# Kernel optimization log

Measured on AMD Instinct MI355X. Metric: run time of the kernel, lower is better.

## Reference

```python
import jax, jax.numpy as jnp
import numpy as np

V, J, NB, NP = 100000, 24, 10, 207
PARENT = np.array([-1, 0, 0, 0, 1, 2, 3, 4, 5, 6, 7, 8, 9, 9, 9, 12, 13, 14, 16, 17, 18, 19, 20, 21])


def setup_inputs() -> dict:
    key = jax.random.key(0)
    ks = jax.random.split(key, 9)
    return {
        "beta": jax.random.normal(ks[0], (NB,), jnp.float32),
        "pose": jax.random.normal(ks[1], (J, 3), jnp.float32),
        "trans": jax.random.normal(ks[2], (3,), jnp.float32),
        "shapedirs": jax.random.normal(ks[3], (V, 3, NB), jnp.float32),
        "v_template": jax.random.normal(ks[4], (V, 3), jnp.float32),
        "J_regressor": jax.random.uniform(ks[5], (J, V), jnp.float32),
        "posedirs": jax.random.normal(ks[6], (V, 3, NP), jnp.float32),
        "weights": jax.random.uniform(ks[7], (V, J), jnp.float32),
        "faces": jax.random.randint(ks[8], (200000, 3), 0, V, jnp.int32),
    }


def _rodrigues(r):
    # r: [N,3] axis-angle -> [N,3,3] rotation matrices
    theta = jnp.sqrt(jnp.sum(r * r, axis=1, keepdims=True)) + 1e-8  # [N,1]
    rh = r / theta
    c = jnp.cos(theta)[:, :, None]  # [N,1,1]
    s = jnp.sin(theta)[:, :, None]
    z = jnp.zeros_like(rh[:, 0])
    K = jnp.stack([z, -rh[:, 2], rh[:, 1],
                   rh[:, 2], z, -rh[:, 0],
                   -rh[:, 1], rh[:, 0], z], axis=1).reshape(-1, 3, 3)
    outer = rh[:, :, None] * rh[:, None, :]
    I = jnp.eye(3, dtype=r.dtype)
    return c * I + (1.0 - c) * outer + s * K


def _with_zeros(Rt):
    # [3,4] -> [4,4] homogeneous
    bottom = jnp.array([[0.0, 0.0, 0.0, 1.0]], dtype=Rt.dtype)
    return jnp.concatenate([Rt, bottom], axis=0)


def reference(beta, pose, trans, shapedirs, v_template, J_regressor, posedirs, weights, faces):
    # shape blending
    v_shaped = jnp.einsum('vdb,b->vd', shapedirs, beta) + v_template  # [V,3]
    Jts = J_regressor @ v_shaped  # [J,3]
    R = _rodrigues(pose)  # [J,3,3]
    # pose blending: lrotmin = (R[1:] - I).flatten(), length 207
    lrotmin = (R[1:] - jnp.eye(3, dtype=R.dtype)).reshape(-1)
    v_posed = v_shaped + jnp.einsum('vdp,p->vd', posedirs, lrotmin)
    # forward kinematics along the 24-joint chain
    G = [_with_zeros(jnp.concatenate([R[0], Jts[0][:, None]], axis=1))]
    for i in range(1, J):
        p = int(PARENT[i])
        loc = _with_zeros(jnp.concatenate([R[i], (Jts[i] - Jts[p])[:, None]], axis=1))
        G.append(G[p] @ loc)
    stacked = jnp.stack(G, axis=0)  # [J,4,4]
    Jh = jnp.concatenate([Jts, jnp.zeros((J, 1), dtype=Jts.dtype)], axis=1)  # [J,4]
    corr = stacked @ Jh[:, :, None]  # [J,4,1]
    A = stacked - jnp.concatenate([jnp.zeros((J, 4, 3), dtype=stacked.dtype), corr], axis=2)
    # LBS skinning
    T = jnp.einsum('vj,jab->vab', weights, A)  # [V,4,4]
    rest = jnp.concatenate([v_posed, jnp.ones((v_posed.shape[0], 1), dtype=v_posed.dtype)], axis=1)  # [V,4]
    v = jnp.einsum('vab,vb->va', T, rest)[:, :3]
    vertices = v + trans[None, :]
    return vertices, faces
```

## Files before the change

kernel.cpp:

```cpp
#include <hip/hip_runtime.h>

#define V_N 100000
#define J_N 24
#define NB_N 10
#define NP_N 207
#define FLAT_P 621
#define FACE_I 600000
#define CHUNKS 50
#define CHUNK_V 2000
#define K1_BLK 1172
#define F_BLK  587

__device__ __constant__ int PARENT_D[24] = {
    -1, 0, 0, 0, 1, 2, 3, 4, 5, 6, 7, 8, 9, 9, 9, 12, 13, 14, 16, 17, 18, 19, 20, 21
};

__device__ __forceinline__ float wave_sum64(float x) {
    float t;
    t = __int_as_float(__builtin_amdgcn_update_dpp(0, __float_as_int(x), 0x111, 0xf, 0xf, true)); x += t;
    t = __int_as_float(__builtin_amdgcn_update_dpp(0, __float_as_int(x), 0x112, 0xf, 0xf, true)); x += t;
    t = __int_as_float(__builtin_amdgcn_update_dpp(0, __float_as_int(x), 0x114, 0xf, 0xf, true)); x += t;
    t = __int_as_float(__builtin_amdgcn_update_dpp(0, __float_as_int(x), 0x118, 0xf, 0xf, true)); x += t;
    t = __int_as_float(__builtin_amdgcn_update_dpp(0, __float_as_int(x), 0x142, 0xa, 0xf, true)); x += t;
    t = __int_as_float(__builtin_amdgcn_update_dpp(0, __float_as_int(x), 0x143, 0xc, 0xf, true)); x += t;
    return __int_as_float(__builtin_amdgcn_readlane(__float_as_int(x), 63));
}

__global__ __launch_bounds__(256) void kA_shape_faces(const float* __restrict__ shapedirs,
                                                      const float* __restrict__ vtemp,
                                                      const float* __restrict__ beta,
                                                      float* __restrict__ vshaped,
                                                      const int4* __restrict__ faces4,
                                                      float* __restrict__ out) {
    int b = blockIdx.x;
    if (b < K1_BLK) {
        int i = b * 256 + threadIdx.x;
        if (i >= V_N * 3) return;
        const float2* sd2 = reinterpret_cast<const float2*>(shapedirs + (size_t)i * NB_N);
        float2 p0 = sd2[0], p1 = sd2[1], p2 = sd2[2], p3 = sd2[3], p4 = sd2[4];
        float acc = vtemp[i];
        acc += p0.x * beta[0] + p0.y * beta[1];
        acc += p1.x * beta[2] + p1.y * beta[3];
        acc += p2.x * beta[4] + p2.y * beta[5];
        acc += p3.x * beta[6] + p3.y * beta[7];
        acc += p4.x * beta[8] + p4.y * beta[9];
        vshaped[i] = acc;
    } else {
        int i = (b - K1_BLK) * 256 + threadIdx.x;
        if (i < FACE_I / 4) {
            int4 f = faces4[i];
            float4* fdst = reinterpret_cast<float4*>(out + 300000);
            fdst[i] = make_float4((float)f.x, (float)f.y, (float)f.z, (float)f.w);
        }
    }
}

__global__ __launch_bounds__(256) void kB_partial(const float* __restrict__ Jreg,
                                                  const float* __restrict__ vshaped,
                                                  float* __restrict__ partials) {
    int c = blockIdx.x, j = blockIdx.y;
    int t = threadIdx.x;
    const float* row = Jreg + (size_t)j * V_N + (size_t)c * CHUNK_V;
    const float* vs  = vshaped + (size_t)c * CHUNK_V * 3;
    float s0 = 0.f, s1 = 0.f, s2 = 0.f;
    for (int i = t; i < CHUNK_V; i += 256) {
        float w = row[i];
        s0 += w * vs[i * 3 + 0];
        s1 += w * vs[i * 3 + 1];
        s2 += w * vs[i * 3 + 2];
    }
    for (int off = 32; off > 0; off >>= 1) {
        s0 += __shfl_xor(s0, off, 64);
        s1 += __shfl_xor(s1, off, 64);
        s2 += __shfl_xor(s2, off, 64);
    }
    __shared__ float ls[3][4];
    int wv = t >> 6;
    if ((t & 63) == 0) { ls[0][wv] = s0; ls[1][wv] = s1; ls[2][wv] = s2; }
    __syncthreads();
    if (t == 0) {
        float* p = partials + (size_t)c * 72 + j * 3;
        p[0] = ls[0][0] + ls[0][1] + ls[0][2] + ls[0][3];
        p[1] = ls[1][0] + ls[1][1] + ls[1][2] + ls[1][3];
        p[2] = ls[2][0] + ls[2][1] + ls[2][2] + ls[2][3];
    }
}

__global__ __launch_bounds__(128) void kC_fk(const float* __restrict__ pose,
                                             const float* __restrict__ partials,
                                             float* __restrict__ ws_lrot,
                                             float* __restrict__ ws_A) {
    __shared__ float R[24][9];
    __shared__ float G[24][12];
    __shared__ float Jts[24][3];
    int t = threadIdx.x;
    if (t < 72) {
        float s = 0.f;
        #pragma unroll
        for (int c = 0; c < CHUNKS; ++c) s += partials[c * 72 + t];
        (&Jts[0][0])[t] = s;
    }
    if (t < 24) {
        float x = pose[t * 3 + 0], y = pose[t * 3 + 1], z = pose[t * 3 + 2];
        float th = sqrtf(x * x + y * y + z * z) + 1e-8f;
        float inv = 1.0f / th;
        float rx = x * inv, ry = y * inv, rz = z * inv;
        float c = cosf(th), s = sinf(th), ic = 1.0f - c;
        R[t][0] = c + ic * rx * rx;      R[t][1] = ic * rx * ry - s * rz;  R[t][2] = ic * rx * rz + s * ry;
        R[t][3] = ic * ry * rx + s * rz; R[t][4] = c + ic * ry * ry;       R[t][5] = ic * ry * rz - s * rx;
        R[t][6] = ic * rz * rx - s * ry; R[t][7] = ic * rz * ry + s * rx;  R[t][8] = c + ic * rz * rz;
    }
    __syncthreads();
    for (int f = t; f < 640; f += 128) {
        float val = 0.0f;
        if (f < FLAT_P) {
            int p = f % NP_N;
            int j = 1 + p / 9;
            int e = p % 9;
            val = R[j][e] - ((e == 0 || e == 4 || e == 8) ? 1.0f : 0.0f);
        }
        ws_lrot[f] = val;
    }
    if (t < 12) {
        int r = t >> 2, c = t & 3;
        G[0][t] = (c < 3) ? R[0][r * 3 + c] : Jts[0][r];
    }
    __syncthreads();
    for (int i = 1; i < J_N; ++i) {
        int p = PARENT_D[i];
        if (t < 12) {
            int r = t >> 2, c = t & 3;
            float sum = (c == 3) ? G[p][r * 4 + 3] : 0.0f;
            #pragma unroll
            for (int k = 0; k < 3; ++k) {
                float loc = (c < 3) ? R[i][k * 3 + c] : (Jts[i][k] - Jts[p][k]);
                sum += G[p][r * 4 + k] * loc;
            }
            G[i][t] = sum;
        }
        __syncthreads();
    }
    if (t < 72) {
        int j = t / 3, r = t % 3;
        float g0 = G[j][r * 4 + 0], g1 = G[j][r * 4 + 1], g2 = G[j][r * 4 + 2], g3 = G[j][r * 4 + 3];
        float corr = g0 * Jts[j][0] + g1 * Jts[j][1] + g2 * Jts[j][2];
        ws_A[j * 12 + r * 4 + 0] = g0;
        ws_A[j * 12 + r * 4 + 1] = g1;
        ws_A[j * 12 + r * 4 + 2] = g2;
        ws_A[j * 12 + r * 4 + 3] = g3 - corr;
    }
}

__global__ __launch_bounds__(256) void kD_main(const float* __restrict__ posedirs,
                                               const float* __restrict__ weights,
                                               const float* __restrict__ vshaped,
                                               const float* __restrict__ ws_lrot,
                                               const float* __restrict__ ws_A,
                                               const float* __restrict__ trans,
                                               float* __restrict__ out) {
    __shared__ float sL[640];
    __shared__ float sA[288];
    int tid = threadIdx.x;
    for (int i = tid; i < 640; i += 256) sL[i] = ws_lrot[i];
    for (int i = tid; i < 288; i += 256) sA[i] = ws_A[i];
    __syncthreads();

    int lane = tid & 63;
    int v = blockIdx.x * 4 + (tid >> 6);
    if (v >= V_N) return;

    const float* pd = posedirs + (size_t)v * FLAT_P;
    float a0 = 0.f, a1 = 0.f, a2 = 0.f;
    #pragma unroll
    for (int k = 0; k < 10; ++k) {
        int f = lane + k * 64;
        if (f < FLAT_P) {
            float val = pd[f] * sL[f];
            if (f < 207)      a0 += val;
            else if (f < 414) a1 += val;
            else              a2 += val;
        }
    }
    float vp0 = wave_sum64(a0) + vshaped[v * 3 + 0];
    float vp1 = wave_sum64(a1) + vshaped[v * 3 + 1];
    float vp2 = wave_sum64(a2) + vshaped[v * 3 + 2];

    float r0 = 0.f, r1 = 0.f, r2 = 0.f;
    if (lane < J_N) {
        float w = weights[(size_t)v * J_N + lane];
        const float* A = &sA[lane * 12];
        r0 = w * (A[0] * vp0 + A[1] * vp1 + A[2]  * vp2 + A[3]);
        r1 = w * (A[4] * vp0 + A[5] * vp1 + A[6]  * vp2 + A[7]);
        r2 = w * (A[8] * vp0 + A[9] * vp1 + A[10] * vp2 + A[11]);
    }
    float s0 = wave_sum64(r0);
    float s1 = wave_sum64(r1);
    float s2 = wave_sum64(r2);

    if (lane < 3) {
        float res = (lane == 0) ? s0 : (lane == 1) ? s1 : s2;
        out[v * 3 + lane] = res + trans[lane];
    }
}

extern "C" void kernel_launch(void* const* d_in, const int* in_sizes, int n_in,
                              void* d_out, int out_size, void* d_ws, size_t ws_size,
                              hipStream_t stream) {
    const float* beta      = (const float*)d_in[0];
    const float* pose      = (const float*)d_in[1];
    const float* trans     = (const float*)d_in[2];
    const float* shapedirs = (const float*)d_in[3];
    const float* v_template= (const float*)d_in[4];
    const float* J_reg     = (const float*)d_in[5];
    const float* posedirs  = (const float*)d_in[6];
    const float* weights   = (const float*)d_in[7];
    const int*   faces     = (const int*)d_in[8];

    float* out = (float*)d_out;

    float* ws       = (float*)d_ws;
    float* vshaped  = ws;
    float* ws_lrot  = ws + 300080;
    float* ws_A     = ws + 300720;
    float* partials = ws + 301008;

    kA_shape_faces<<<K1_BLK + F_BLK, 256, 0, stream>>>(shapedirs, v_template, beta, vshaped,
                                                       (const int4*)faces, out);
    kB_partial<<<dim3(CHUNKS, J_N), 256, 0, stream>>>(J_reg, vshaped, partials);
    kC_fk<<<1, 128, 0, stream>>>(pose, partials, ws_lrot, ws_A);
    kD_main<<<(V_N + 3) / 4, 256, 0, stream>>>(posedirs, weights, vshaped, ws_lrot, ws_A, trans, out);
}
```

Baseline: 84.87 us.

## Split pose-blend and skinning into separate thread-per-element kernels

```diff
diff --git a/kernel.cpp b/kernel.cpp
--- a/kernel.cpp
+++ b/kernel.cpp
@@ -14,17 +14,6 @@
 __device__ __constant__ int PARENT_D[24] = {
     -1, 0, 0, 0, 1, 2, 3, 4, 5, 6, 7, 8, 9, 9, 9, 12, 13, 14, 16, 17, 18, 19, 20, 21
 };
-
-__device__ __forceinline__ float wave_sum64(float x) {
-    float t;
-    t = __int_as_float(__builtin_amdgcn_update_dpp(0, __float_as_int(x), 0x111, 0xf, 0xf, true)); x += t;
-    t = __int_as_float(__builtin_amdgcn_update_dpp(0, __float_as_int(x), 0x112, 0xf, 0xf, true)); x += t;
-    t = __int_as_float(__builtin_amdgcn_update_dpp(0, __float_as_int(x), 0x114, 0xf, 0xf, true)); x += t;
-    t = __int_as_float(__builtin_amdgcn_update_dpp(0, __float_as_int(x), 0x118, 0xf, 0xf, true)); x += t;
-    t = __int_as_float(__builtin_amdgcn_update_dpp(0, __float_as_int(x), 0x142, 0xa, 0xf, true)); x += t;
-    t = __int_as_float(__builtin_amdgcn_update_dpp(0, __float_as_int(x), 0x143, 0xc, 0xf, true)); x += t;
-    return __int_as_float(__builtin_amdgcn_readlane(__float_as_int(x), 63));
-}
 
 __global__ __launch_bounds__(256) void kA_shape_faces(const float* __restrict__ shapedirs,
                                                       const float* __restrict__ vtemp,
@@ -151,56 +140,55 @@
     }
 }
 
-__global__ __launch_bounds__(256) void kD_main(const float* __restrict__ posedirs,
-                                               const float* __restrict__ weights,
-                                               const float* __restrict__ vshaped,
-                                               const float* __restrict__ ws_lrot,
-                                               const float* __restrict__ ws_A,
-                                               const float* __restrict__ trans,
-                                               float* __restrict__ out) {
-    __shared__ float sL[640];
+__global__ __launch_bounds__(256) void kD1_blend(const float* __restrict__ posedirs,
+                                                 const float* __restrict__ vshaped,
+                                                 const float* __restrict__ ws_lrot,
+                                                 float* __restrict__ vp) {
+    __shared__ float sL[NP_N];
+    int tid = threadIdx.x;
+    if (tid < NP_N) sL[tid] = ws_lrot[tid];
+    __syncthreads();
+
+    int i = blockIdx.x * 256 + tid;
+    if (i >= V_N * 3) return;
+
+    const float* pd = posedirs + (size_t)i * NP_N;
+    float acc = 0.f;
+    #pragma unroll 9
+    for (int j = 0; j < NP_N; ++j) {
+        acc += pd[j] * sL[j];
+    }
+    vp[i] = acc + vshaped[i];
+}
+
+__global__ __launch_bounds__(256) void kD2_skin(const float* __restrict__ weights,
+                                                const float* __restrict__ vp,
+                                                const float* __restrict__ ws_A,
+                                                const float* __restrict__ trans,
+                                                float* __restrict__ out) {
     __shared__ float sA[288];
     int tid = threadIdx.x;
-    for (int i = tid; i < 640; i += 256) sL[i] = ws_lrot[i];
     for (int i = tid; i < 288; i += 256) sA[i] = ws_A[i];
     __syncthreads();
 
-    int lane = tid & 63;
-    int v = blockIdx.x * 4 + (tid >> 6);
+    int v = blockIdx.x * 256 + tid;
     if (v >= V_N) return;
 
-    const float* pd = posedirs + (size_t)v * FLAT_P;
-    float a0 = 0.f, a1 = 0.f, a2 = 0.f;
+    const float* wv = weights + (size_t)v * J_N;
+    float T[12];
     #pragma unroll
-    for (int k = 0; k < 10; ++k) {
-        int f = lane + k * 64;
-        if (f < FLAT_P) {
-            float val = pd[f] * sL[f];
-            if (f < 207)      a0 += val;
-            else if (f < 414) a1 += val;
-            else              a2 += val;
-        }
-    }
-    float vp0 = wave_sum64(a0) + vshaped[v * 3 + 0];
-    float vp1 = wave_sum64(a1) + vshaped[v * 3 + 1];
-    float vp2 = wave_sum64(a2) + vshaped[v * 3 + 2];
-
-    float r0 = 0.f, r1 = 0.f, r2 = 0.f;
-    if (lane < J_N) {
-        float w = weights[(size_t)v * J_N + lane];
-        const float* A = &sA[lane * 12];
-        r0 = w * (A[0] * vp0 + A[1] * vp1 + A[2]  * vp2 + A[3]);
-        r1 = w * (A[4] * vp0 + A[5] * vp1 + A[6]  * vp2 + A[7]);
-        r2 = w * (A[8] * vp0 + A[9] * vp1 + A[10] * vp2 + A[11]);
-    }
-    float s0 = wave_sum64(r0);
-    float s1 = wave_sum64(r1);
-    float s2 = wave_sum64(r2);
-
-    if (lane < 3) {
-        float res = (lane == 0) ? s0 : (lane == 1) ? s1 : s2;
-        out[v * 3 + lane] = res + trans[lane];
-    }
+    for (int e = 0; e < 12; ++e) T[e] = 0.f;
+    #pragma unroll
+    for (int j = 0; j < J_N; ++j) {
+        float wgt = wv[j];
+        const float* A = &sA[j * 12];
+        #pragma unroll
+        for (int e = 0; e < 12; ++e) T[e] += wgt * A[e];
+    }
+    float vp0 = vp[v * 3 + 0], vp1 = vp[v * 3 + 1], vp2 = vp[v * 3 + 2];
+    out[v * 3 + 0] = T[0] * vp0 + T[1] * vp1 + T[2]  * vp2 + T[3]  + trans[0];
+    out[v * 3 + 1] = T[4] * vp0 + T[5] * vp1 + T[6]  * vp2 + T[7]  + trans[1];
+    out[v * 3 + 2] = T[8] * vp0 + T[9] * vp1 + T[10] * vp2 + T[11] + trans[2];
 }
 
 extern "C" void kernel_launch(void* const* d_in, const int* in_sizes, int n_in,
@@ -223,10 +211,12 @@
     float* ws_lrot  = ws + 300080;
     float* ws_A     = ws + 300720;
     float* partials = ws + 301008;
+    float* vp       = ws + 310000;
 
     kA_shape_faces<<<K1_BLK + F_BLK, 256, 0, stream>>>(shapedirs, v_template, beta, vshaped,
                                                        (const int4*)faces, out);
     kB_partial<<<dim3(CHUNKS, J_N), 256, 0, stream>>>(J_reg, vshaped, partials);
     kC_fk<<<1, 128, 0, stream>>>(pose, partials, ws_lrot, ws_A);
-    kD_main<<<(V_N + 3) / 4, 256, 0, stream>>>(posedirs, weights, vshaped, ws_lrot, ws_A, trans, out);
-}
+    kD1_blend<<<(V_N * 3 + 255) / 256, 256, 0, stream>>>(posedirs, vshaped, ws_lrot, vp);
+    kD2_skin<<<(V_N + 255) / 256, 256, 0, stream>>>(weights, vp, ws_A, trans, out);
+}
```

Result: slower. 129.6 us (+52.7%).
